# Performance work log

Measured on AMD Instinct MI355X. Metric: run time of the kernel, lower is better.

## Reference

```python
import jax, jax.numpy as jnp
import numpy as np

N, E = 100000, 1600000
D_IN, D_HID, D_OUT = 128, 128, 64
EPS_BN = 1e-5
EPS_NORM = 1e-12


def setup_inputs() -> dict:
    key = jax.random.key(0)
    ks = jax.random.split(key, 16)
    x = jax.random.normal(ks[0], (N, D_IN), jnp.float32)
    edge_index = jax.random.randint(ks[1], (2, E), 0, N, dtype=jnp.int32)
    edge_weight = jax.random.uniform(ks[2], (E,), jnp.float32)

    def lin_w(k, fan_in, fan_out):  # Glorot-ish init
        return jax.random.normal(k, (fan_in, fan_out), jnp.float32) / np.sqrt(fan_in).astype(np.float32)

    inp = dict(x=x, edge_index=edge_index, edge_weight=edge_weight)
    inp["W1"] = lin_w(ks[3], D_IN, D_HID)
    inp["b1"] = jnp.zeros((D_HID,), jnp.float32)
    inp["g1"] = jnp.ones((D_HID,), jnp.float32)
    inp["be1"] = jnp.zeros((D_HID,), jnp.float32)
    inp["rm1"] = 0.1 * jax.random.normal(ks[4], (D_HID,), jnp.float32)
    inp["rv1"] = 0.5 + jax.random.uniform(ks[5], (D_HID,), jnp.float32)
    inp["W2"] = lin_w(ks[6], D_HID, D_HID)
    inp["b2"] = jnp.zeros((D_HID,), jnp.float32)
    inp["g2"] = jnp.ones((D_HID,), jnp.float32)
    inp["be2"] = jnp.zeros((D_HID,), jnp.float32)
    inp["rm2"] = 0.1 * jax.random.normal(ks[7], (D_HID,), jnp.float32)
    inp["rv2"] = 0.5 + jax.random.uniform(ks[8], (D_HID,), jnp.float32)
    inp["W3"] = lin_w(ks[9], D_HID, D_OUT)
    inp["b3"] = jnp.zeros((D_OUT,), jnp.float32)
    return inp


def _gcn_conv(x, row, col, w, W, b):
    # symmetric normalization: deg from target nodes (col), PyG GCNConv default
    deg = jax.ops.segment_sum(w, col, num_segments=N)  # [N]
    deg_safe = jnp.where(deg > 0, deg, 1.0)
    dinv = jnp.where(deg > 0, jax.lax.rsqrt(deg_safe), 0.0)
    norm = dinv[row] * w * dinv[col]                   # [E+N]
    xw = x @ W                                          # [N, out]
    msg = xw[row] * norm[:, None]                       # gather + scale
    out = jax.ops.segment_sum(msg, col, num_segments=N)  # scatter-add
    return out + b


def _bn(x, g, be, rm, rv):  # eval-mode BatchNorm
    return (x - rm) * jax.lax.rsqrt(rv + EPS_BN) * g + be


def reference(x, edge_index, edge_weight,
              W1, b1, g1, be1, rm1, rv1,
              W2, b2, g2, be2, rm2, rv2,
              W3, b3):
    loop = jnp.arange(N, dtype=edge_index.dtype)
    row = jnp.concatenate([edge_index[0], loop])  # self-loops appended
    col = jnp.concatenate([edge_index[1], loop])
    w = jnp.concatenate([edge_weight, jnp.ones((N,), edge_weight.dtype)])

    h = _gcn_conv(x, row, col, w, W1, b1)
    h = jax.nn.relu(_bn(h, g1, be1, rm1, rv1))  # dropout is no-op in eval
    h = _gcn_conv(h, row, col, w, W2, b2)
    h = jax.nn.relu(_bn(h, g2, be2, rm2, rv2))
    h = _gcn_conv(h, row, col, w, W3, b3)
    nrm = jnp.linalg.norm(h, axis=1, keepdims=True)
    return h / jnp.maximum(nrm, EPS_NORM)  # F.normalize(p=2, dim=1)
```

## Files before the change

### kernel.cpp

```cpp
#include <hip/hip_runtime.h>
#include <cstddef>

#define TPB 256
#define AB_CHUNK 4096

typedef __attribute__((ext_vector_type(8))) short short8;
typedef __attribute__((ext_vector_type(4))) float f32x4;

__device__ inline unsigned short f2bf(float f) {
  unsigned int u = __float_as_uint(f);
  return (unsigned short)((u + 0x7fffu + ((u >> 16) & 1u)) >> 16);
}
__device__ inline float bflo(unsigned int u) { return __uint_as_float(u << 16); }
__device__ inline float bfhi(unsigned int u) { return __uint_as_float(u & 0xffff0000u); }

__global__ __launch_bounds__(256) void histA(const int* __restrict__ col,
                                             int* __restrict__ cntmat,
                                             int E, int nbk, int nblkA) {
  __shared__ int hist[512];
  for (int i = threadIdx.x; i < nbk; i += 256) hist[i] = 0;
  __syncthreads();
  const int base = blockIdx.x * AB_CHUNK;
  const int lim  = min(base + AB_CHUNK, E);
  for (int i = base + threadIdx.x; i < lim; i += 256)
    atomicAdd(&hist[col[i] >> 8], 1);
  __syncthreads();
  for (int k = threadIdx.x; k < nbk; k += 256)
    cntmat[k * nblkA + blockIdx.x] = hist[k];
}

__global__ __launch_bounds__(256) void scan_partial(const int* __restrict__ cnt,
                                                    int* __restrict__ bsum, int n) {
  __shared__ int red[256];
  const int b = blockIdx.x, tid = threadIdx.x;
  const int base = b * 1024 + tid * 4;
  int s = 0;
  if (base + 3 < n) {
    int4 v = *(const int4*)(cnt + base);
    s = v.x + v.y + v.z + v.w;
  } else {
    for (int j = 0; j < 4; ++j) if (base + j < n) s += cnt[base + j];
  }
  red[tid] = s; __syncthreads();
  for (int off = 128; off >= 1; off >>= 1) {
    if (tid < off) red[tid] += red[tid + off];
    __syncthreads();
  }
  if (tid == 0) bsum[b] = red[0];
}

__global__ __launch_bounds__(1024) void scan_bsum(int* __restrict__ bsum, int nb,
                                                  int* __restrict__ out, int n) {
  __shared__ int sh[1024];
  const int tid = threadIdx.x;
  int v = (tid < nb) ? bsum[tid] : 0;
  sh[tid] = v; __syncthreads();
  for (int off = 1; off < 1024; off <<= 1) {
    int t = (tid >= off) ? sh[tid - off] : 0;
    __syncthreads();
    sh[tid] += t;
    __syncthreads();
  }
  if (tid < nb) bsum[tid] = sh[tid] - v;
  if (tid == 1023) out[n] = sh[1023];
}

__global__ __launch_bounds__(256) void scan_apply(const int* __restrict__ cnt,
                                                  const int* __restrict__ bsum,
                                                  int* __restrict__ out, int n) {
  __shared__ int red[256];
  const int b = blockIdx.x, tid = threadIdx.x;
  const int base = b * 1024 + tid * 4;
  int v0 = 0, v1 = 0, v2 = 0, v3 = 0;
  if (base + 3 < n) {
    int4 v = *(const int4*)(cnt + base);
    v0 = v.x; v1 = v.y; v2 = v.z; v3 = v.w;
  } else {
    if (base     < n) v0 = cnt[base];
    if (base + 1 < n) v1 = cnt[base + 1];
    if (base + 2 < n) v2 = cnt[base + 2];
    if (base + 3 < n) v3 = cnt[base + 3];
  }
  const int t = v0 + v1 + v2 + v3;
  red[tid] = t; __syncthreads();
  for (int off = 1; off < 256; off <<= 1) {
    int x = (tid >= off) ? red[tid - off] : 0;
    __syncthreads();
    red[tid] += x;
    __syncthreads();
  }
  int excl = red[tid] - t + bsum[b];
  if (base     < n) out[base]     = excl;
  if (base + 1 < n) out[base + 1] = excl + v0;
  if (base + 2 < n) out[base + 2] = excl + v0 + v1;
  if (base + 3 < n) out[base + 3] = excl + v0 + v1 + v2;
}

__global__ __launch_bounds__(256) void scatA(const int* __restrict__ row,
                                             const int* __restrict__ col,
                                             const float* __restrict__ w,
                                             const int* __restrict__ scnt,
                                             int2* __restrict__ bucketed,
                                             int E, int nbk, int nblkA) {
  __shared__ int cur[512];
  for (int k = threadIdx.x; k < nbk; k += 256)
    cur[k] = scnt[k * nblkA + blockIdx.x];
  __syncthreads();
  const int base = blockIdx.x * AB_CHUNK;
  const int lim  = min(base + AB_CHUNK, E);
  for (int i = base + threadIdx.x; i < lim; i += 256) {
    int c = col[i];
    int pos = atomicAdd(&cur[c >> 8], 1);
    bucketed[pos] = make_int2(row[i] | ((c & 255) << 17), __float_as_int(w[i]));
  }
}

__global__ __launch_bounds__(256) void bucketB(const int2* __restrict__ bucketed,
                                               const int* __restrict__ scnt,
                                               int2* __restrict__ csr,
                                               int* __restrict__ rowptr,
                                               float* __restrict__ dinv,
                                               int E, int N, int nbk, int nblkA) {
  __shared__ int   hist[256];
  __shared__ float degf[256];
  __shared__ int   excl[256];
  const int b = blockIdx.x, tid = threadIdx.x;
  const int start = scnt[b * nblkA];
  const int end   = (b == nbk - 1) ? E : scnt[(b + 1) * nblkA];
  hist[tid] = 0; degf[tid] = 0.f;
  __syncthreads();
  for (int i = start + tid; i < end; i += 256) {
    int2 p = bucketed[i];
    int cl = (p.x >> 17) & 255;
    atomicAdd(&hist[cl], 1);
    atomicAdd(&degf[cl], __int_as_float(p.y));
  }
  __syncthreads();
  const int v = hist[tid];
  excl[tid] = v;
  __syncthreads();
  for (int off = 1; off < 256; off <<= 1) {
    int t = (tid >= off) ? excl[tid - off] : 0;
    __syncthreads();
    excl[tid] += t;
    __syncthreads();
  }
  const int ex = excl[tid] - v;
  const int node = b * 256 + tid;
  if (node < N) {
    rowptr[node] = start + ex;
    dinv[node]   = rsqrtf(degf[tid] + 1.0f);
  }
  if (b == nbk - 1 && tid == 0) rowptr[N] = E;
  __syncthreads();
  hist[tid] = ex;
  __syncthreads();
  for (int i = start + tid; i < end; i += 256) {
    int2 p = bucketed[i];
    int cl = (p.x >> 17) & 255;
    int pos = start + atomicAdd(&hist[cl], 1);
    csr[pos] = make_int2(p.x & 0x1FFFF, p.y);
  }
}

__global__ void bn_prep_kernel(const float* g1, const float* be1, const float* rm1, const float* rv1,
                               const float* g2, const float* be2, const float* rm2, const float* rv2,
                               float* sc1, float* sh1, float* sc2, float* sh2) {
  int t = threadIdx.x;
  if (t < 128) {
    float s1 = g1[t] * rsqrtf(rv1[t] + 1e-5f);
    sc1[t] = s1; sh1[t] = be1[t] - rm1[t] * s1;
    float s2 = g2[t] * rsqrtf(rv2[t] + 1e-5f);
    sc2[t] = s2; sh2[t] = be2[t] - rm2[t] * s2;
  }
}

__global__ void wt_kernel(const float* __restrict__ W, unsigned short* __restrict__ Wt, int DOUT) {
  int t = blockIdx.x * blockDim.x + threadIdx.x;
  int nidx = t >> 7, k = t & 127;
  Wt[t] = f2bf(W[(size_t)k * DOUT + nidx]);
}

template<int DOUT, bool BF16IN>
__global__ __launch_bounds__(256) void gemm_mfma(
    const void* Xin,
    const unsigned short* __restrict__ Wt,
    const float* __restrict__ dinv,
    unsigned int* __restrict__ XWb, int n)
{
  constexpr int CT = DOUT / 16;
  __shared__ unsigned short Xs[64][136];
  __shared__ unsigned short Ws[DOUT][136];
  const int tid = threadIdx.x;
  const int r0  = blockIdx.x * 64;

  if constexpr (BF16IN) {
    const unsigned int* hb = (const unsigned int*)Xin;
    for (int i = tid; i < 64 * 16; i += 256) {
      int rr = i >> 4, q = i & 15;
      uint4 v = make_uint4(0, 0, 0, 0);
      if (r0 + rr < n) v = *(const uint4*)(hb + (size_t)(r0 + rr) * 64 + q * 4);
      *(uint4*)(&Xs[rr][q * 8]) = v;
    }
  } else {
    const float* X = (const float*)Xin;
    for (int i = tid; i < 64 * 32; i += 256) {
      int rr = i >> 5, q = i & 31;
      float4 v = make_float4(0.f, 0.f, 0.f, 0.f);
      if (r0 + rr < n) v = *(const float4*)(X + (size_t)(r0 + rr) * 128 + q * 4);
      uint2 p;
      p.x = (unsigned)f2bf(v.x) | ((unsigned)f2bf(v.y) << 16);
      p.y = (unsigned)f2bf(v.z) | ((unsigned)f2bf(v.w) << 16);
      *(uint2*)(&Xs[rr][q * 4]) = p;
    }
  }
  for (int i = tid; i < DOUT * 16; i += 256) {
    int nr = i >> 4, q = i & 15;
    *(uint4*)(&Ws[nr][q * 8]) = *(const uint4*)(Wt + (size_t)nr * 128 + q * 8);
  }
  __syncthreads();

  const int wid  = tid >> 6, lane = tid & 63;
  const int arow = wid * 16 + (lane & 15);
  const int koff = (lane >> 4) << 3;

  short8 af[4];
#pragma unroll
  for (int s = 0; s < 4; ++s)
    af[s] = *(const short8*)(&Xs[arow][s * 32 + koff]);

  f32x4 acc[CT];
#pragma unroll
  for (int ct = 0; ct < CT; ++ct) acc[ct] = (f32x4){0.f, 0.f, 0.f, 0.f};

#pragma unroll
  for (int ct = 0; ct < CT; ++ct) {
    const int brow = ct * 16 + (lane & 15);
#pragma unroll
    for (int s = 0; s < 4; ++s) {
      short8 bf = *(const short8*)(&Ws[brow][s * 32 + koff]);
      acc[ct] = __builtin_amdgcn_mfma_f32_16x16x32_bf16(af[s], bf, acc[ct], 0, 0, 0);
    }
  }

  const int rbase = r0 + wid * 16 + ((lane >> 4) << 2);
  float dvv[4];
#pragma unroll
  for (int i = 0; i < 4; ++i) dvv[i] = (rbase + i < n) ? dinv[rbase + i] : 0.f;

#pragma unroll
  for (int ct = 0; ct < CT; ++ct) {
#pragma unroll
    for (int i = 0; i < 4; ++i) {
      float v = acc[ct][i] * dvv[i];
      float o = __shfl_xor(v, 1);
      if (!(lane & 1) && rbase + i < n) {
        unsigned int p = (unsigned)f2bf(v) | ((unsigned)f2bf(o) << 16);
        XWb[(size_t)(rbase + i) * (DOUT / 2) + ct * 8 + ((lane & 15) >> 1)] = p;
      }
    }
  }
}

template<int D, int MODE>
__global__ __launch_bounds__(256) void gather_kernel(
    const int* __restrict__ rowptr, const int2* __restrict__ csr,
    const unsigned int* __restrict__ xwb, const float* __restrict__ dinv,
    const float* __restrict__ bias,
    const float* __restrict__ bnsc, const float* __restrict__ bnsh,
    void* __restrict__ outp, int n)
{
  int wid  = (blockIdx.x * blockDim.x + threadIdx.x) >> 6;
  int lane = threadIdx.x & 63;
  if (wid >= n) return;
  const int start = rowptr[wid];
  const int end   = rowptr[wid + 1];
  const float dv  = dinv[wid];

  if constexpr (MODE == 0) {
    unsigned int su = xwb[(size_t)wid * 64 + lane];
    float a0 = bflo(su), a1 = bfhi(su);
    int e = start;
    for (; e + 3 < end; e += 4) {
      int2 p0 = csr[e], p1 = csr[e + 1], p2 = csr[e + 2], p3 = csr[e + 3];
      unsigned int u0 = xwb[(size_t)p0.x * 64 + lane];
      unsigned int u1 = xwb[(size_t)p1.x * 64 + lane];
      unsigned int u2 = xwb[(size_t)p2.x * 64 + lane];
      unsigned int u3 = xwb[(size_t)p3.x * 64 + lane];
      float n0 = __int_as_float(p0.y), n1 = __int_as_float(p1.y);
      float n2 = __int_as_float(p2.y), n3 = __int_as_float(p3.y);
      a0 = fmaf(bflo(u0), n0, a0); a1 = fmaf(bfhi(u0), n0, a1);
      a0 = fmaf(bflo(u1), n1, a0); a1 = fmaf(bfhi(u1), n1, a1);
      a0 = fmaf(bflo(u2), n2, a0); a1 = fmaf(bfhi(u2), n2, a1);
      a0 = fmaf(bflo(u3), n3, a0); a1 = fmaf(bfhi(u3), n3, a1);
    }
    for (; e < end; ++e) {
      int2 p0 = csr[e];
      unsigned int u0 = xwb[(size_t)p0.x * 64 + lane];
      float n0 = __int_as_float(p0.y);
      a0 = fmaf(bflo(u0), n0, a0); a1 = fmaf(bfhi(u0), n0, a1);
    }
    a0 = fmaf(dv, a0, bias[lane * 2]);
    a1 = fmaf(dv, a1, bias[lane * 2 + 1]);
    a0 = fmaxf(fmaf(a0, bnsc[lane * 2],     bnsh[lane * 2]),     0.f);
    a1 = fmaxf(fmaf(a1, bnsc[lane * 2 + 1], bnsh[lane * 2 + 1]), 0.f);
    ((unsigned int*)outp)[(size_t)wid * 64 + lane] =
        (unsigned)f2bf(a0) | ((unsigned)f2bf(a1) << 16);
  } else {
    const int ui = lane >> 1;
    unsigned int su = xwb[(size_t)wid * 32 + ui];
    float a = (lane & 1) ? bfhi(su) : bflo(su);
    int e = start;
    for (; e + 3 < end; e += 4) {
      int2 p0 = csr[e], p1 = csr[e + 1], p2 = csr[e + 2], p3 = csr[e + 3];
      unsigned int u0 = xwb[(size_t)p0.x * 32 + ui];
      unsigned int u1 = xwb[(size_t)p1.x * 32 + ui];
      unsigned int u2 = xwb[(size_t)p2.x * 32 + ui];
      unsigned int u3 = xwb[(size_t)p3.x * 32 + ui];
      float v0 = (lane & 1) ? bfhi(u0) : bflo(u0);
      float v1 = (lane & 1) ? bfhi(u1) : bflo(u1);
      float v2 = (lane & 1) ? bfhi(u2) : bflo(u2);
      float v3 = (lane & 1) ? bfhi(u3) : bflo(u3);
      a = fmaf(v0, __int_as_float(p0.y), a);
      a = fmaf(v1, __int_as_float(p1.y), a);
      a = fmaf(v2, __int_as_float(p2.y), a);
      a = fmaf(v3, __int_as_float(p3.y), a);
    }
    for (; e < end; ++e) {
      int2 p0 = csr[e];
      unsigned int u0 = xwb[(size_t)p0.x * 32 + ui];
      float v0 = (lane & 1) ? bfhi(u0) : bflo(u0);
      a = fmaf(v0, __int_as_float(p0.y), a);
    }
    a = fmaf(dv, a, bias[lane]);
    float s = a * a;
#pragma unroll
    for (int off = 32; off >= 1; off >>= 1) s += __shfl_xor(s, off);
    float scale = 1.0f / fmaxf(sqrtf(s), 1e-12f);
    ((float*)outp)[(size_t)wid * 64 + lane] = a * scale;
  }
}

extern "C" void kernel_launch(void* const* d_in, const int* in_sizes, int n_in,
                              void* d_out, int out_size, void* d_ws, size_t ws_size,
                              hipStream_t stream)
{
  const float* x   = (const float*)d_in[0];
  const int*   ei  = (const int*)d_in[1];
  const float* ew  = (const float*)d_in[2];
  const float* W1  = (const float*)d_in[3];
  const float* b1  = (const float*)d_in[4];
  const float* g1  = (const float*)d_in[5];
  const float* be1 = (const float*)d_in[6];
  const float* rm1 = (const float*)d_in[7];
  const float* rv1 = (const float*)d_in[8];
  const float* W2  = (const float*)d_in[9];
  const float* b2  = (const float*)d_in[10];
  const float* g2  = (const float*)d_in[11];
  const float* be2 = (const float*)d_in[12];
  const float* rm2 = (const float*)d_in[13];
  const float* rv2 = (const float*)d_in[14];
  const float* W3  = (const float*)d_in[15];
  const float* b3  = (const float*)d_in[16];

  const int N = in_sizes[0] / 128;
  const int E = in_sizes[2];
  const int* row = ei;
  const int* col = ei + E;

  const int nbk   = (N + 255) >> 8;
  const int nblkA = (E + AB_CHUNK - 1) / AB_CHUNK;
  const int L     = nbk * nblkA;
  const int nb2   = (L + 1023) / 1024;

  char* ws = (char*)d_ws;
  size_t off = 0;
  auto alloc = [&](size_t bytes) -> void* {
    void* p = ws + off;
    off += (bytes + 255) & ~(size_t)255;
    return p;
  };
  int*   cntmat = (int*)  alloc((size_t)L * 4);
  int*   scnt   = (int*)  alloc((size_t)(L + 1) * 4);
  int*   bsum   = (int*)  alloc((size_t)1024 * 4);
  int2*  bucketed = (int2*)alloc((size_t)E * 8);
  int2*  csr    = (int2*) alloc((size_t)E * 8);
  int*   rowptr = (int*)  alloc((size_t)(N + 1) * 4);
  float* dinv   = (float*)alloc((size_t)N * 4);
  float* sc1    = (float*)alloc(512);
  float* sh1    = (float*)alloc(512);
  float* sc2    = (float*)alloc(512);
  float* sh2    = (float*)alloc(512);
  unsigned short* Wt1 = (unsigned short*)alloc(128 * 128 * 2);
  unsigned short* Wt2 = (unsigned short*)alloc(128 * 128 * 2);
  unsigned short* Wt3 = (unsigned short*)alloc(64 * 128 * 2);
  unsigned int* xwb = (unsigned int*)alloc((size_t)N * 64 * 4);
  unsigned int* hb  = (unsigned int*)alloc((size_t)N * 64 * 4);

  wt_kernel<<<64, 256, 0, stream>>>(W1, Wt1, 128);
  wt_kernel<<<64, 256, 0, stream>>>(W2, Wt2, 128);
  wt_kernel<<<32, 256, 0, stream>>>(W3, Wt3, 64);
  bn_prep_kernel<<<1, 128, 0, stream>>>(g1, be1, rm1, rv1, g2, be2, rm2, rv2,
                                        sc1, sh1, sc2, sh2);

  histA<<<nblkA, 256, 0, stream>>>(col, cntmat, E, nbk, nblkA);
  scan_partial<<<nb2, 256, 0, stream>>>(cntmat, bsum, L);
  scan_bsum<<<1, 1024, 0, stream>>>(bsum, nb2, scnt, L);
  scan_apply<<<nb2, 256, 0, stream>>>(cntmat, bsum, scnt, L);
  scatA<<<nblkA, 256, 0, stream>>>(row, col, ew, scnt, bucketed, E, nbk, nblkA);
  bucketB<<<nbk, 256, 0, stream>>>(bucketed, scnt, csr, rowptr, dinv, E, N, nbk, nblkA);

  const int gGM = (N + 63) / 64;
  const int gW  = (N + 3) / 4;

  gemm_mfma<128, false><<<gGM, 256, 0, stream>>>(x, Wt1, dinv, xwb, N);
  gather_kernel<128, 0><<<gW, 256, 0, stream>>>(rowptr, csr, xwb, dinv, b1, sc1, sh1, hb, N);

  gemm_mfma<128, true><<<gGM, 256, 0, stream>>>(hb, Wt2, dinv, xwb, N);
  gather_kernel<128, 0><<<gW, 256, 0, stream>>>(rowptr, csr, xwb, dinv, b2, sc2, sh2, hb, N);

  gemm_mfma<64, true><<<gGM, 256, 0, stream>>>(hb, Wt3, dinv, xwb, N);
  gather_kernel<64, 1><<<gW, 256, 0, stream>>>(rowptr, csr, xwb, dinv, b3, nullptr, nullptr,
                                               (float*)d_out, N);
}
```

Measured before the change: 357.5 us.

## Slice feature matrices by column for cache-local gathers and pack CSR entries

The XW and hidden buffers are stored in 8 column slices of 32 bytes (or 16 bytes) per node. Each gather block handles one slice, so its random neighbour reads hit a smaller working set that fits in L2, and a wave processes several edges in parallel. CSR entries are packed into 32 bits (17-bit row index plus a 15-bit bf16 weight with the sign bit dropped), which halves index traffic but rounds edge weights to bf16. The last layer now writes partial squared sums and needs an extra normalisation kernel. The three weight-transpose launches are merged into one.

```diff
diff --git a/kernel.cpp b/kernel.cpp
--- a/kernel.cpp
+++ b/kernel.cpp
@@ -117,7 +117,7 @@
 
 __global__ __launch_bounds__(256) void bucketB(const int2* __restrict__ bucketed,
                                                const int* __restrict__ scnt,
-                                               int2* __restrict__ csr,
+                                               unsigned int* __restrict__ csr4,
                                                int* __restrict__ rowptr,
                                                float* __restrict__ dinv,
                                                int E, int N, int nbk, int nblkA) {
@@ -159,7 +159,8 @@
     int2 p = bucketed[i];
     int cl = (p.x >> 17) & 255;
     int pos = start + atomicAdd(&hist[cl], 1);
-    csr[pos] = make_int2(p.x & 0x1FFFF, p.y);
+    unsigned int wq = (unsigned int)f2bf(__int_as_float(p.y)) & 0x7fffu;
+    csr4[pos] = ((unsigned int)(p.x & 0x1FFFF) << 15) | wq;
   }
 }
 
@@ -175,10 +176,21 @@
   }
 }
 
-__global__ void wt_kernel(const float* __restrict__ W, unsigned short* __restrict__ Wt, int DOUT) {
+__global__ void wt3_kernel(const float* __restrict__ W1, const float* __restrict__ W2,
+                           const float* __restrict__ W3,
+                           unsigned short* __restrict__ Wt1, unsigned short* __restrict__ Wt2,
+                           unsigned short* __restrict__ Wt3) {
   int t = blockIdx.x * blockDim.x + threadIdx.x;
-  int nidx = t >> 7, k = t & 127;
-  Wt[t] = f2bf(W[(size_t)k * DOUT + nidx]);
+  if (t < 16384) {
+    int nidx = t >> 7, k = t & 127;
+    Wt1[t] = f2bf(W1[(size_t)k * 128 + nidx]);
+  } else if (t < 32768) {
+    int u = t - 16384; int nidx = u >> 7, k = u & 127;
+    Wt2[u] = f2bf(W2[(size_t)k * 128 + nidx]);
+  } else if (t < 40960) {
+    int u = t - 32768; int nidx = u >> 7, k = u & 127;
+    Wt3[u] = f2bf(W3[(size_t)k * 64 + nidx]);
+  }
 }
 
 template<int DOUT, bool BF16IN>
@@ -195,12 +207,13 @@
   const int r0  = blockIdx.x * 64;
 
   if constexpr (BF16IN) {
-    const unsigned int* hb = (const unsigned int*)Xin;
+    const unsigned int* hbs = (const unsigned int*)Xin;
     for (int i = tid; i < 64 * 16; i += 256) {
-      int rr = i >> 4, q = i & 15;
+      int rr = i >> 4, s = (i >> 1) & 7, hf = i & 1;
       uint4 v = make_uint4(0, 0, 0, 0);
-      if (r0 + rr < n) v = *(const uint4*)(hb + (size_t)(r0 + rr) * 64 + q * 4);
-      *(uint4*)(&Xs[rr][q * 8]) = v;
+      if (r0 + rr < n)
+        v = *(const uint4*)(hbs + ((size_t)s * n + (r0 + rr)) * 8 + hf * 4);
+      *(uint4*)(&Xs[rr][s * 16 + hf * 8]) = v;
     }
   } else {
     const float* X = (const float*)Xin;
@@ -256,89 +269,94 @@
       float o = __shfl_xor(v, 1);
       if (!(lane & 1) && rbase + i < n) {
         unsigned int p = (unsigned)f2bf(v) | ((unsigned)f2bf(o) << 16);
-        XWb[(size_t)(rbase + i) * (DOUT / 2) + ct * 8 + ((lane & 15) >> 1)] = p;
+        int cp = ct * 8 + ((lane & 15) >> 1);
+        if constexpr (DOUT == 128)
+          XWb[((size_t)(cp >> 3) * n + (rbase + i)) * 8 + (cp & 7)] = p;
+        else
+          XWb[((size_t)(cp >> 2) * n + (rbase + i)) * 4 + (cp & 3)] = p;
       }
     }
   }
 }
 
-template<int D, int MODE>
+template<int SLICE_U, int MODE>
 __global__ __launch_bounds__(256) void gather_kernel(
-    const int* __restrict__ rowptr, const int2* __restrict__ csr,
-    const unsigned int* __restrict__ xwb, const float* __restrict__ dinv,
+    const int* __restrict__ rowptr, const unsigned int* __restrict__ csr4,
+    const unsigned int* __restrict__ xwbs, const float* __restrict__ dinv,
     const float* __restrict__ bias,
     const float* __restrict__ bnsc, const float* __restrict__ bnsh,
-    void* __restrict__ outp, int n)
+    void* __restrict__ outp, float* __restrict__ psum, int n)
 {
-  int wid  = (blockIdx.x * blockDim.x + threadIdx.x) >> 6;
-  int lane = threadIdx.x & 63;
-  if (wid >= n) return;
-  const int start = rowptr[wid];
-  const int end   = rowptr[wid + 1];
-  const float dv  = dinv[wid];
+  const int slice = blockIdx.x & 7;
+  const int node  = (int)(blockIdx.x >> 3) * 4 + (int)(threadIdx.x >> 6);
+  const int lane  = threadIdx.x & 63;
+  if (node >= n) return;
+  const int start = rowptr[node];
+  const int end   = rowptr[node + 1];
+  const float dv  = dinv[node];
+  constexpr int LPE   = SLICE_U / 2;
+  constexpr int NSLOT = 64 / LPE;
+  const int li = lane & (LPE - 1);
+  const int es = lane / LPE;
+  const unsigned int* base = xwbs + (size_t)slice * n * SLICE_U;
+
+  float a0 = 0.f, a1 = 0.f, a2 = 0.f, a3 = 0.f;
+  for (int e = start; e < end; e += NSLOT) {
+    int idx = e + es;
+    bool valid = idx < end;
+    unsigned int c = csr4[valid ? idx : start];
+    int r = (int)(c >> 15);
+    float nm = valid ? __uint_as_float((c & 0x7fffu) << 16) : 0.f;
+    uint2 u = *(const uint2*)(base + (size_t)r * SLICE_U + li * 2);
+    a0 = fmaf(bflo(u.x), nm, a0); a1 = fmaf(bfhi(u.x), nm, a1);
+    a2 = fmaf(bflo(u.y), nm, a2); a3 = fmaf(bfhi(u.y), nm, a3);
+  }
+#pragma unroll
+  for (int off = LPE; off < 64; off <<= 1) {
+    a0 += __shfl_xor(a0, off); a1 += __shfl_xor(a1, off);
+    a2 += __shfl_xor(a2, off); a3 += __shfl_xor(a3, off);
+  }
+  uint2 su = *(const uint2*)(base + (size_t)node * SLICE_U + li * 2);
+  a0 += bflo(su.x); a1 += bfhi(su.x); a2 += bflo(su.y); a3 += bfhi(su.y);
+  const int f = slice * (SLICE_U * 2) + li * 4;
+  a0 = fmaf(dv, a0, bias[f]);     a1 = fmaf(dv, a1, bias[f + 1]);
+  a2 = fmaf(dv, a2, bias[f + 2]); a3 = fmaf(dv, a3, bias[f + 3]);
 
   if constexpr (MODE == 0) {
-    unsigned int su = xwb[(size_t)wid * 64 + lane];
-    float a0 = bflo(su), a1 = bfhi(su);
-    int e = start;
-    for (; e + 3 < end; e += 4) {
-      int2 p0 = csr[e], p1 = csr[e + 1], p2 = csr[e + 2], p3 = csr[e + 3];
-      unsigned int u0 = xwb[(size_t)p0.x * 64 + lane];
-      unsigned int u1 = xwb[(size_t)p1.x * 64 + lane];
-      unsigned int u2 = xwb[(size_t)p2.x * 64 + lane];
-      unsigned int u3 = xwb[(size_t)p3.x * 64 + lane];
-      float n0 = __int_as_float(p0.y), n1 = __int_as_float(p1.y);
-      float n2 = __int_as_float(p2.y), n3 = __int_as_float(p3.y);
-      a0 = fmaf(bflo(u0), n0, a0); a1 = fmaf(bfhi(u0), n0, a1);
-      a0 = fmaf(bflo(u1), n1, a0); a1 = fmaf(bfhi(u1), n1, a1);
-      a0 = fmaf(bflo(u2), n2, a0); a1 = fmaf(bfhi(u2), n2, a1);
-      a0 = fmaf(bflo(u3), n3, a0); a1 = fmaf(bfhi(u3), n3, a1);
-    }
-    for (; e < end; ++e) {
-      int2 p0 = csr[e];
-      unsigned int u0 = xwb[(size_t)p0.x * 64 + lane];
-      float n0 = __int_as_float(p0.y);
-      a0 = fmaf(bflo(u0), n0, a0); a1 = fmaf(bfhi(u0), n0, a1);
-    }
-    a0 = fmaf(dv, a0, bias[lane * 2]);
-    a1 = fmaf(dv, a1, bias[lane * 2 + 1]);
-    a0 = fmaxf(fmaf(a0, bnsc[lane * 2],     bnsh[lane * 2]),     0.f);
-    a1 = fmaxf(fmaf(a1, bnsc[lane * 2 + 1], bnsh[lane * 2 + 1]), 0.f);
-    ((unsigned int*)outp)[(size_t)wid * 64 + lane] =
-        (unsigned)f2bf(a0) | ((unsigned)f2bf(a1) << 16);
+    a0 = fmaxf(fmaf(a0, bnsc[f],     bnsh[f]),     0.f);
+    a1 = fmaxf(fmaf(a1, bnsc[f + 1], bnsh[f + 1]), 0.f);
+    a2 = fmaxf(fmaf(a2, bnsc[f + 2], bnsh[f + 2]), 0.f);
+    a3 = fmaxf(fmaf(a3, bnsc[f + 3], bnsh[f + 3]), 0.f);
+    if (es == 0) {
+      uint2 p;
+      p.x = (unsigned)f2bf(a0) | ((unsigned)f2bf(a1) << 16);
+      p.y = (unsigned)f2bf(a2) | ((unsigned)f2bf(a3) << 16);
+      *(uint2*)((unsigned int*)outp + ((size_t)slice * n + node) * SLICE_U + li * 2) = p;
+    }
   } else {
-    const int ui = lane >> 1;
-    unsigned int su = xwb[(size_t)wid * 32 + ui];
-    float a = (lane & 1) ? bfhi(su) : bflo(su);
-    int e = start;
-    for (; e + 3 < end; e += 4) {
-      int2 p0 = csr[e], p1 = csr[e + 1], p2 = csr[e + 2], p3 = csr[e + 3];
-      unsigned int u0 = xwb[(size_t)p0.x * 32 + ui];
-      unsigned int u1 = xwb[(size_t)p1.x * 32 + ui];
-      unsigned int u2 = xwb[(size_t)p2.x * 32 + ui];
-      unsigned int u3 = xwb[(size_t)p3.x * 32 + ui];
-      float v0 = (lane & 1) ? bfhi(u0) : bflo(u0);
-      float v1 = (lane & 1) ? bfhi(u1) : bflo(u1);
-      float v2 = (lane & 1) ? bfhi(u2) : bflo(u2);
-      float v3 = (lane & 1) ? bfhi(u3) : bflo(u3);
-      a = fmaf(v0, __int_as_float(p0.y), a);
-      a = fmaf(v1, __int_as_float(p1.y), a);
-      a = fmaf(v2, __int_as_float(p2.y), a);
-      a = fmaf(v3, __int_as_float(p3.y), a);
-    }
-    for (; e < end; ++e) {
-      int2 p0 = csr[e];
-      unsigned int u0 = xwb[(size_t)p0.x * 32 + ui];
-      float v0 = (lane & 1) ? bfhi(u0) : bflo(u0);
-      a = fmaf(v0, __int_as_float(p0.y), a);
-    }
-    a = fmaf(dv, a, bias[lane]);
-    float s = a * a;
-#pragma unroll
-    for (int off = 32; off >= 1; off >>= 1) s += __shfl_xor(s, off);
-    float scale = 1.0f / fmaxf(sqrtf(s), 1e-12f);
-    ((float*)outp)[(size_t)wid * 64 + lane] = a * scale;
-  }
+    float s = a0 * a0 + a1 * a1 + a2 * a2 + a3 * a3;
+    s += __shfl_xor(s, 1);
+    if (lane == 0) psum[(size_t)slice * n + node] = s;
+    if (es == 0) {
+      float4 o = make_float4(a0, a1, a2, a3);
+      *(float4*)((float*)outp + ((size_t)slice * n + node) * 8 + li * 4) = o;
+    }
+  }
+}
+
+__global__ __launch_bounds__(256) void norm_kernel(const float* __restrict__ h3,
+                                                   const float* __restrict__ psum,
+                                                   float* __restrict__ out, int n) {
+  int t = blockIdx.x * 256 + threadIdx.x;
+  int node = t >> 6, lane = t & 63;
+  if (node >= n) return;
+  float part = psum[(size_t)(lane & 7) * n + node];
+  part += __shfl_xor(part, 1);
+  part += __shfl_xor(part, 2);
+  part += __shfl_xor(part, 4);
+  int slice = lane >> 3, f = lane & 7;
+  float v = h3[((size_t)slice * n + node) * 8 + f];
+  out[(size_t)node * 64 + lane] = v / fmaxf(sqrtf(part), 1e-12f);
 }
 
 extern "C" void kernel_launch(void* const* d_in, const int* in_sizes, int n_in,
@@ -384,7 +402,7 @@
   int*   scnt   = (int*)  alloc((size_t)(L + 1) * 4);
   int*   bsum   = (int*)  alloc((size_t)1024 * 4);
   int2*  bucketed = (int2*)alloc((size_t)E * 8);
-  int2*  csr    = (int2*) alloc((size_t)E * 8);
+  unsigned int* csr4 = (unsigned int*)alloc((size_t)E * 4);
   int*   rowptr = (int*)  alloc((size_t)(N + 1) * 4);
   float* dinv   = (float*)alloc((size_t)N * 4);
   float* sc1    = (float*)alloc(512);
@@ -396,10 +414,10 @@
   unsigned short* Wt3 = (unsigned short*)alloc(64 * 128 * 2);
   unsigned int* xwb = (unsigned int*)alloc((size_t)N * 64 * 4);
   unsigned int* hb  = (unsigned int*)alloc((size_t)N * 64 * 4);
-
-  wt_kernel<<<64, 256, 0, stream>>>(W1, Wt1, 128);
-  wt_kernel<<<64, 256, 0, stream>>>(W2, Wt2, 128);
-  wt_kernel<<<32, 256, 0, stream>>>(W3, Wt3, 64);
+  float* h3   = (float*)alloc((size_t)N * 64 * 4);
+  float* psum = (float*)alloc((size_t)N * 8 * 4);
+
+  wt3_kernel<<<160, 256, 0, stream>>>(W1, W2, W3, Wt1, Wt2, Wt3);
   bn_prep_kernel<<<1, 128, 0, stream>>>(g1, be1, rm1, rv1, g2, be2, rm2, rv2,
                                         sc1, sh1, sc2, sh2);
 
@@ -408,18 +426,19 @@
   scan_bsum<<<1, 1024, 0, stream>>>(bsum, nb2, scnt, L);
   scan_apply<<<nb2, 256, 0, stream>>>(cntmat, bsum, scnt, L);
   scatA<<<nblkA, 256, 0, stream>>>(row, col, ew, scnt, bucketed, E, nbk, nblkA);
-  bucketB<<<nbk, 256, 0, stream>>>(bucketed, scnt, csr, rowptr, dinv, E, N, nbk, nblkA);
+  bucketB<<<nbk, 256, 0, stream>>>(bucketed, scnt, csr4, rowptr, dinv, E, N, nbk, nblkA);
 
   const int gGM = (N + 63) / 64;
-  const int gW  = (N + 3) / 4;
+  const int gW  = ((N + 3) / 4) * 8;
+  const int gNm = (N * 64 + 255) / 256;
 
   gemm_mfma<128, false><<<gGM, 256, 0, stream>>>(x, Wt1, dinv, xwb, N);
-  gather_kernel<128, 0><<<gW, 256, 0, stream>>>(rowptr, csr, xwb, dinv, b1, sc1, sh1, hb, N);
+  gather_kernel<8, 0><<<gW, 256, 0, stream>>>(rowptr, csr4, xwb, dinv, b1, sc1, sh1, hb, nullptr, N);
 
   gemm_mfma<128, true><<<gGM, 256, 0, stream>>>(hb, Wt2, dinv, xwb, N);
-  gather_kernel<128, 0><<<gW, 256, 0, stream>>>(rowptr, csr, xwb, dinv, b2, sc2, sh2, hb, N);
+  gather_kernel<8, 0><<<gW, 256, 0, stream>>>(rowptr, csr4, xwb, dinv, b2, sc2, sh2, hb, nullptr, N);
 
   gemm_mfma<64, true><<<gGM, 256, 0, stream>>>(hb, Wt3, dinv, xwb, N);
-  gather_kernel<64, 1><<<gW, 256, 0, stream>>>(rowptr, csr, xwb, dinv, b3, nullptr, nullptr,
-                                               (float*)d_out, N);
-}
+  gather_kernel<4, 1><<<gW, 256, 0, stream>>>(rowptr, csr4, xwb, dinv, b3, nullptr, nullptr, h3, psum, N);
+  norm_kernel<<<gNm, 256, 0, stream>>>(h3, psum, (float*)d_out, N);
+}
```

Result: slower. 779.6 us (+118.0%).
